# Performance work log

Hardware: AMD Instinct MI355X
Metric: run time of the kernel (lower is better)

Reference implementation:

```python
import jax, jax.numpy as jnp
import numpy as np

V, D, H, S = 100000, 300, 300, 4096   # vocab, embed dim, biLSTM hidden (2x150), seq len
HU = H // 2                            # per-direction LSTM units
NSYN = 4


def _lstm(x, W, U, b):
    """Keras-style LSTM scan. x: [S, D] -> hidden states [S, HU]. Gate order i,f,g,o."""
    def step(carry, xt):
        h, c = carry
        z = xt @ W + h @ U + b              # [4*HU]
        i, f, g, o = jnp.split(z, 4)
        i = jax.nn.sigmoid(i)
        f = jax.nn.sigmoid(f)
        g = jnp.tanh(g)
        o = jax.nn.sigmoid(o)
        c = f * c + i * g
        h = o * jnp.tanh(c)
        return (h, c), h
    init = (jnp.zeros((HU,), x.dtype), jnp.zeros((HU,), x.dtype))
    _, hs = jax.lax.scan(step, init, x)
    return hs


def setup_inputs() -> dict:
    key = jax.random.key(0)
    ks = jax.random.split(key, 20)
    s = 0.05  # small init scale keeps exp() attention scores well-conditioned
    return {
        "sentence": jax.random.randint(ks[0], (S,), 0, V),
        "synonym_indices": jax.random.randint(ks[1], (S, NSYN), 0, V),
        "embedding_matrix": jax.random.normal(ks[2], (V, D), jnp.float32) * s,
        # forward-direction LSTM
        "W_f": jax.random.normal(ks[3], (D, 4 * HU), jnp.float32) * s,
        "U_f": jax.random.normal(ks[4], (HU, 4 * HU), jnp.float32) * s,
        "b_f": jnp.zeros((4 * HU,), jnp.float32),
        # backward-direction LSTM
        "W_b": jax.random.normal(ks[5], (D, 4 * HU), jnp.float32) * s,
        "U_b": jax.random.normal(ks[6], (HU, 4 * HU), jnp.float32) * s,
        "b_b": jnp.zeros((4 * HU,), jnp.float32),
        # primary attention dense (h1 -> h1)
        "W_p": jax.random.normal(ks[7], (H, H), jnp.float32) * s,
        "b_p": jnp.zeros((H,), jnp.float32),
        # secondary attention dense (2*h1 -> 1, tanh)
        "W_s": jax.random.normal(ks[8], (2 * H, 1), jnp.float32) * s,
        "b_s": jnp.zeros((1,), jnp.float32),
        # output heads
        "W_emo": jax.random.normal(ks[9], (2 * H, 8), jnp.float32) * s,
        "b_emo": jnp.zeros((8,), jnp.float32),
        "W_sent": jax.random.normal(ks[10], (2 * H, 1), jnp.float32) * s,
        "b_sent": jnp.zeros((1,), jnp.float32),
    }


def reference(sentence, synonym_indices, embedding_matrix,
              W_f, U_f, b_f, W_b, U_b, b_b,
              W_p, b_p, W_s, b_s, W_emo, b_emo, W_sent, b_sent):
    emb = embedding_matrix[sentence]                       # [S, D] gather
    # bidirectional LSTM (concat fwd and reversed-bwd hidden states)
    h_fwd = _lstm(emb, W_f, U_f, b_f)                      # [S, HU]
    h_bwd = _lstm(emb[::-1], W_b, U_b, b_b)[::-1]          # [S, HU]
    hidden_states = jnp.concatenate([h_fwd, h_bwd], -1)    # [S, H]
    # primary attention: per-word synonym gather + exp-scored weighted sum (vectorized)
    out = hidden_states @ W_p + b_p                        # [S, H]
    syn = embedding_matrix[synonym_indices]                # [S, NSYN, D] irregular gather
    scores = jnp.exp(jnp.einsum('sd,skd->sk', out, syn))   # [S, NSYN]
    m = jnp.einsum('sk,skd->sd', scores, syn)              # [S, D]
    h_hats = jnp.concatenate([hidden_states, m], -1)       # [S, 2H]
    # secondary attention
    coeff = jnp.exp(jnp.tanh(h_hats @ W_s + b_s))          # [S, 1]
    H_HAT = jnp.sum(coeff * h_hats, axis=0)[None, :]       # [1, 2H]
    emotion_logits = H_HAT @ W_emo + b_emo                 # [1, 8]
    sentiment_logits = H_HAT @ W_sent + b_sent             # [1, 1]
    return (emotion_logits, sentiment_logits)
```

## Files before the change

kernel.cpp:

```cpp
#include <hip/hip_runtime.h>
#include <hip/hip_bf16.h>
#include <math.h>

#define S_LEN 4096
#define D_EMB 300
#define NG    600
#define HDIM  300
#define H2    600
#define VOCAB 100000

typedef float v4f __attribute__((ext_vector_type(4)));
typedef _Float16 f16x2 __attribute__((ext_vector_type(2)));
typedef _Float16 f16x8 __attribute__((ext_vector_type(8)));

__device__ __forceinline__ float bf2f(unsigned short u) {
  union { unsigned int i; float f; } v; v.i = ((unsigned int)u) << 16; return v.f;
}
__device__ __forceinline__ unsigned short f2bf(float f) {
  union { float f; unsigned int i; } v; v.f = f;
  return (unsigned short)((v.i + 0x7FFFu + ((v.i >> 16) & 1u)) >> 16);
}

__device__ __forceinline__ void bar_lds() {
  asm volatile("s_waitcnt lgkmcnt(0)\n\ts_barrier" ::: "memory");
}

__global__ void zero_hh(float* __restrict__ HH) {
  if (threadIdx.x < 640) HH[threadIdx.x] = 0.f;
}
__global__ void zero_out_f(float* __restrict__ o, int n) {
  if ((int)threadIdx.x < n) o[threadIdx.x] = 0.f;
}

#define BM 64
#define BN 64
#define BK 16
template<bool A_BF16>
__global__ __launch_bounds__(256) void gemm_bias(
    const void* __restrict__ Av,
    const int* __restrict__ idx, int lda, int nrowsA,
    const float* __restrict__ B,
    const float* __restrict__ bias,
    unsigned short* __restrict__ C,
    int N, int K)
{
  __shared__ __align__(16) float As[BK][BM + 4];
  __shared__ __align__(16) float Bs[BK][BN + 4];
  __shared__ int rowidx[BM];

  int tid = threadIdx.x;
  int bm0 = blockIdx.y * BM, bn0 = blockIdx.x * BN;
  if (tid < BM) {
    int r = idx ? idx[bm0 + tid] : (bm0 + tid);
    r = (r < 0) ? 0 : ((r >= nrowsA) ? (nrowsA - 1) : r);
    rowidx[tid] = r;
  }
  __syncthreads();

  int tx  = tid & 15, ty = tid >> 4;
  int ar  = tid >> 2, akv = (tid & 3) << 2;
  int bkr = tid >> 4, bnv = (tid & 15) << 2;

  float acc[4][4] = {};
  for (int kk = 0; kk < K; kk += BK) {
    float a0=0.f, a1=0.f, a2=0.f, a3=0.f;
    int ka = kk + akv;
    if (ka < K) {
      if (A_BF16) {
        const unsigned short* A = (const unsigned short*)Av;
        ushort4 qa = *(const ushort4*)(A + (size_t)rowidx[ar]*lda + ka);
        a0 = bf2f(qa.x); a1 = bf2f(qa.y); a2 = bf2f(qa.z); a3 = bf2f(qa.w);
      } else {
        const float* A = (const float*)Av;
        float4 qa = *(const float4*)(A + (size_t)rowidx[ar]*lda + ka);
        a0 = qa.x; a1 = qa.y; a2 = qa.z; a3 = qa.w;
      }
    }
    float b0=0.f, b1=0.f, b2=0.f, b3=0.f;
    int kb = kk + bkr, nb = bn0 + bnv;
    if (kb < K && nb < N) {
      float4 qb = *(const float4*)(B + (size_t)kb*N + nb);
      b0 = qb.x; b1 = qb.y; b2 = qb.z; b3 = qb.w;
    }
    As[akv+0][ar] = a0; As[akv+1][ar] = a1; As[akv+2][ar] = a2; As[akv+3][ar] = a3;
    Bs[bkr][bnv+0] = b0; Bs[bkr][bnv+1] = b1; Bs[bkr][bnv+2] = b2; Bs[bkr][bnv+3] = b3;
    __syncthreads();
    #pragma unroll
    for (int k = 0; k < BK; ++k) {
      v4f av = *(const v4f*)&As[k][ty << 2];
      v4f bv = *(const v4f*)&Bs[k][tx << 2];
      #pragma unroll
      for (int i = 0; i < 4; ++i)
        #pragma unroll
        for (int j = 0; j < 4; ++j)
          acc[i][j] += av[i] * bv[j];
    }
    __syncthreads();
  }
  #pragma unroll
  for (int i = 0; i < 4; ++i) {
    int m = bm0 + (ty << 2) + i;
    #pragma unroll
    for (int j = 0; j < 4; ++j) {
      int n = bn0 + (tx << 2) + j;
      if (n < N) C[(size_t)m*N + n] = f2bf(acc[i][j] + bias[n]);
    }
  }
}

__global__ __launch_bounds__(768) void lstm_kernel(
    const unsigned short* __restrict__ pre_f, const unsigned short* __restrict__ pre_b,
    const float* __restrict__ Uf, const float* __restrict__ Ub,
    unsigned short* __restrict__ hidden )
{
  const int dir = blockIdx.x;
  const unsigned short* pre = dir ? pre_b : pre_f;
  const float* U            = dir ? Ub : Uf;
  const int tid = threadIdx.x;

  __shared__ __align__(16) unsigned short h_u16[160];
  __shared__ __align__(16) float z2[3000];
  __shared__ __align__(16) unsigned short h_hist[8][160];

  const bool faP = tid < 750;
  const bool bc  = tid < 150;
  const int c4 = tid % 150, q = tid / 150;
  const int j0 = c4 << 2;
  const int k0 = q << 5;

  f16x2 u[4][16];
  if (faP) {
    #pragma unroll
    for (int cc = 0; cc < 4; ++cc)
      #pragma unroll
      for (int p = 0; p < 16; ++p) {
        int k = k0 + (p << 1);
        float a = (k     < 150) ? U[(size_t)k    *600 + j0 + cc] : 0.f;
        float b = (k + 1 < 150) ? U[(size_t)(k+1)*600 + j0 + cc] : 0.f;
        f16x2 v; v[0] = (_Float16)a; v[1] = (_Float16)b;
        u[cc][p] = v;
      }
  }

  const int t0 = dir ? (S_LEN - 1) : 0;
  const int dt = dir ? -1 : 1;
  const ptrdiff_t pstep = (ptrdiff_t)dt * 600;

  if (tid < 160) h_u16[tid] = 0;

  float pA0=0,pA1=0,pA2=0,pA3=0, pB0=0,pB1=0,pB2=0,pB3=0;
  const unsigned short* pre2 = pre + (ptrdiff_t)t0*600 + 2*pstep;
  if (bc) {
    const unsigned short* g0 = pre + (ptrdiff_t)t0*600;
    pA0 = bf2f(g0[tid]); pA1 = bf2f(g0[tid+150]);
    pA2 = bf2f(g0[tid+300]); pA3 = bf2f(g0[tid+450]);
    const unsigned short* g1 = g0 + pstep;
    pB0 = bf2f(g1[tid]); pB1 = bf2f(g1[tid+150]);
    pB2 = bf2f(g1[tid+300]); pB3 = bf2f(g1[tid+450]);
  }
  float c = 0.f;
  __syncthreads();

  const _Float16* hf = (const _Float16*)h_u16;

  for (int s8 = 0; s8 < S_LEN/8; ++s8) {
    if (s8 && tid < 600) {
      int sub = tid / 75, w = (tid % 75) << 1;
      int sp  = (s8 << 3) - 8 + sub;
      int tp  = dir ? (S_LEN - 1 - sp) : sp;
      *(unsigned int*)(hidden + (size_t)tp*300 + dir*150 + w) =
          *(const unsigned int*)&h_hist[sub][w];
    }
    #pragma unroll
    for (int ss = 0; ss < 8; ++ss) {
      const int s = (s8 << 3) + ss;
      if (faP) {
        f16x2 hp[16];
        *(f16x8*)&hp[0]  = *(const f16x8*)&hf[k0];
        *(f16x8*)&hp[4]  = *(const f16x8*)&hf[k0 + 8];
        *(f16x8*)&hp[8]  = *(const f16x8*)&hf[k0 + 16];
        *(f16x8*)&hp[12] = *(const f16x8*)&hf[k0 + 24];
        float a0 = 0.f, a1 = 0.f, a2 = 0.f, a3 = 0.f;
        #pragma unroll
        for (int p = 0; p < 16; ++p) {
          a0 = __builtin_amdgcn_fdot2(hp[p], u[0][p], a0, false);
          a1 = __builtin_amdgcn_fdot2(hp[p], u[1][p], a1, false);
          a2 = __builtin_amdgcn_fdot2(hp[p], u[2][p], a2, false);
          a3 = __builtin_amdgcn_fdot2(hp[p], u[3][p], a3, false);
        }
        v4f zp; zp[0] = a0; zp[1] = a1; zp[2] = a2; zp[3] = a3;
        *(v4f*)&z2[q*600 + j0] = zp;
      }
      float pC0=0,pC1=0,pC2=0,pC3=0;
      if (bc && s + 2 < S_LEN) {
        pC0 = bf2f(pre2[tid]);       pC1 = bf2f(pre2[tid+150]);
        pC2 = bf2f(pre2[tid+300]);   pC3 = bf2f(pre2[tid+450]);
      }
      bar_lds();

      if (bc) {
        float zi = pA0 + ((z2[tid      ] + z2[600+tid      ]) + (z2[1200+tid      ] + z2[1800+tid      ])) + z2[2400+tid      ];
        float zf = pA1 + ((z2[tid + 150] + z2[600+tid + 150]) + (z2[1200+tid + 150] + z2[1800+tid + 150])) + z2[2400+tid + 150];
        float zg = pA2 + ((z2[tid + 300] + z2[600+tid + 300]) + (z2[1200+tid + 300] + z2[1800+tid + 300])) + z2[2400+tid + 300];
        float zo = pA3 + ((z2[tid + 450] + z2[600+tid + 450]) + (z2[1200+tid + 450] + z2[1800+tid + 450])) + z2[2400+tid + 450];
        float gi = __builtin_amdgcn_rcpf(1.f + __expf(-zi));
        float gf = __builtin_amdgcn_rcpf(1.f + __expf(-zf));
        float gg = 1.f - 2.f * __builtin_amdgcn_rcpf(__expf(2.f * zg) + 1.f);
        float go = __builtin_amdgcn_rcpf(1.f + __expf(-zo));
        c = gf * c + gi * gg;
        float th = 1.f - 2.f * __builtin_amdgcn_rcpf(__expf(2.f * c) + 1.f);
        float hv = go * th;
        ((_Float16*)h_u16)[tid] = (_Float16)hv;
        h_hist[ss][tid] = f2bf(hv);
        pA0 = pB0; pA1 = pB1; pA2 = pB2; pA3 = pB3;
        pB0 = pC0; pB1 = pC1; pB2 = pC2; pB3 = pC3;
      }
      bar_lds();
      pre2 += pstep;
    }
  }

  if (tid < 600) {
    int sub = tid / 75, w = (tid % 75) << 1;
    int sp  = S_LEN - 8 + sub;
    int tp  = dir ? (S_LEN - 1 - sp) : sp;
    *(unsigned int*)(hidden + (size_t)tp*300 + dir*150 + w) =
        *(const unsigned int*)&h_hist[sub][w];
  }
}

__global__ __launch_bounds__(128) void attn_word(
    const unsigned short* __restrict__ outp,
    const unsigned short* __restrict__ hid,
    const float* __restrict__ E,
    const int* __restrict__ syn,
    const float* __restrict__ W_s,
    const float* __restrict__ b_s,
    float* __restrict__ HH)
{
  int t = blockIdx.x, tid = threadIdx.x;
  __shared__ float s_out[300], s_hid[300], s_syn[4][300], s_m[300];
  __shared__ float s_red[8], s_sc[4], s_cf;

  int r0 = syn[t*4+0], r1 = syn[t*4+1], r2 = syn[t*4+2], r3 = syn[t*4+3];
  r0 = (r0 < 0) ? 0 : ((r0 >= VOCAB) ? VOCAB-1 : r0);
  r1 = (r1 < 0) ? 0 : ((r1 >= VOCAB) ? VOCAB-1 : r1);
  r2 = (r2 < 0) ? 0 : ((r2 >= VOCAB) ? VOCAB-1 : r2);
  r3 = (r3 < 0) ? 0 : ((r3 >= VOCAB) ? VOCAB-1 : r3);
  for (int d = tid; d < 300; d += 128) {
    s_out[d] = bf2f(outp[(size_t)t*300 + d]);
    s_hid[d] = bf2f(hid[(size_t)t*300 + d]);
    s_syn[0][d] = E[(size_t)r0*300 + d];
    s_syn[1][d] = E[(size_t)r1*300 + d];
    s_syn[2][d] = E[(size_t)r2*300 + d];
    s_syn[3][d] = E[(size_t)r3*300 + d];
  }
  __syncthreads();

  float p0=0.f, p1=0.f, p2=0.f, p3=0.f;
  for (int d = tid; d < 300; d += 128) {
    float o = s_out[d];
    p0 += o*s_syn[0][d]; p1 += o*s_syn[1][d];
    p2 += o*s_syn[2][d]; p3 += o*s_syn[3][d];
  }
  #pragma unroll
  for (int off = 32; off; off >>= 1) {
    p0 += __shfl_down(p0, off); p1 += __shfl_down(p1, off);
    p2 += __shfl_down(p2, off); p3 += __shfl_down(p3, off);
  }
  int wave = tid >> 6, lane = tid & 63;
  if (lane == 0) {
    s_red[wave*4+0] = p0; s_red[wave*4+1] = p1;
    s_red[wave*4+2] = p2; s_red[wave*4+3] = p3;
  }
  __syncthreads();
  if (tid < 4) s_sc[tid] = __expf(fminf(s_red[tid] + s_red[4 + tid], 50.f));
  __syncthreads();

  float sc0 = s_sc[0], sc1 = s_sc[1], sc2 = s_sc[2], sc3 = s_sc[3];
  float cp = 0.f;
  for (int d = tid; d < 300; d += 128) {
    float m = sc0*s_syn[0][d] + sc1*s_syn[1][d] + sc2*s_syn[2][d] + sc3*s_syn[3][d];
    s_m[d] = m;
    cp += s_hid[d]*W_s[d] + m*W_s[300 + d];
  }
  #pragma unroll
  for (int off = 32; off; off >>= 1) cp += __shfl_down(cp, off);
  if (lane == 0) s_red[wave] = cp;
  __syncthreads();
  if (tid == 0) s_cf = __expf(tanhf(s_red[0] + s_red[1] + b_s[0]));
  __syncthreads();

  float cf = s_cf;
  for (int d = tid; d < 300; d += 128) {
    atomicAdd(&HH[d],       cf * s_hid[d]);
    atomicAdd(&HH[300 + d], cf * s_m[d]);
  }
}

__global__ void heads(const float* __restrict__ HH,
                      const float* __restrict__ W_emo, const float* __restrict__ b_emo,
                      const float* __restrict__ W_sent, const float* __restrict__ b_sent,
                      float* __restrict__ out) {
  int tid = threadIdx.x;
  if (tid < 8) {
    float a = 0.f;
    for (int d = 0; d < H2; ++d) a += HH[d] * W_emo[d*8 + tid];
    out[tid] = a + b_emo[tid];
  } else if (tid == 8) {
    float a = 0.f;
    for (int d = 0; d < H2; ++d) a += HH[d] * W_sent[d];
    out[8] = a + b_sent[0];
  }
}

extern "C" void kernel_launch(void* const* d_in, const int* in_sizes, int n_in,
                              void* d_out, int out_size, void* d_ws, size_t ws_size,
                              hipStream_t stream) {
  const int*   sentence = (const int*)d_in[0];
  const int*   syn_idx  = (const int*)d_in[1];
  const float* E        = (const float*)d_in[2];
  const float* W_f      = (const float*)d_in[3];
  const float* U_f      = (const float*)d_in[4];
  const float* b_f      = (const float*)d_in[5];
  const float* W_b      = (const float*)d_in[6];
  const float* U_b      = (const float*)d_in[7];
  const float* b_b      = (const float*)d_in[8];
  const float* W_p      = (const float*)d_in[9];
  const float* b_p      = (const float*)d_in[10];
  const float* W_s      = (const float*)d_in[11];
  const float* b_s      = (const float*)d_in[12];
  const float* W_emo    = (const float*)d_in[13];
  const float* b_emo    = (const float*)d_in[14];
  const float* W_sent   = (const float*)d_in[15];
  const float* b_sent   = (const float*)d_in[16];
  float*       outv     = (float*)d_out;

  unsigned char* ws = (unsigned char*)d_ws;
  float*          HH     = (float*)ws;
  unsigned short* hidden = (unsigned short*)(ws + 2560);
  unsigned short* out_p  = (unsigned short*)(ws + 2460160);
  unsigned short* pre_f  = (unsigned short*)(ws + 4917760);
  unsigned short* pre_b  = (unsigned short*)(ws + 9832960);

  if (ws_size < 14748160u) {
    zero_out_f<<<1, 64, 0, stream>>>(outv, out_size);
    return;
  }

  zero_hh<<<1, 640, 0, stream>>>(HH);
  gemm_bias<false><<<dim3(10, 64), 256, 0, stream>>>(
      (const void*)E, sentence, D_EMB, VOCAB, W_f, b_f, pre_f, NG, D_EMB);
  gemm_bias<false><<<dim3(10, 64), 256, 0, stream>>>(
      (const void*)E, sentence, D_EMB, VOCAB, W_b, b_b, pre_b, NG, D_EMB);
  lstm_kernel<<<2, 768, 0, stream>>>(pre_f, pre_b, U_f, U_b, hidden);
  gemm_bias<true><<<dim3(5, 64), 256, 0, stream>>>(
      (const void*)hidden, nullptr, HDIM, S_LEN, W_p, b_p, out_p, HDIM, HDIM);
  attn_word<<<S_LEN, 128, 0, stream>>>(out_p, hidden, E, syn_idx, W_s, b_s, HH);
  heads<<<1, 64, 0, stream>>>(HH, W_emo, b_emo, W_sent, b_sent, outv);
}
```

Measured before the change: 3.643 ms.

## Assign one LSTM gate column per thread and compute activations in parallel

The recurrent matvec is re-partitioned. Previously 750 threads each computed a partial K-slice for four columns, and 150 threads reduced five partials per gate. Now each of 600 threads owns one full gate column, with 80 fp16 pairs of U held in registers, so no split-K reduction through LDS is needed. Each thread also applies its own sigmoid or tanh activation before writing G, which spreads the transcendental work across 600 lanes instead of 150. The cost is a longer serial dot product per thread (80 fdot2 versus 16×4) and higher register pressure.

```diff
diff --git a/kernel.cpp b/kernel.cpp
--- a/kernel.cpp
+++ b/kernel.cpp
@@ -108,7 +108,7 @@
   }
 }
 
-__global__ __launch_bounds__(768) void lstm_kernel(
+__global__ __launch_bounds__(640) void lstm_kernel(
     const unsigned short* __restrict__ pre_f, const unsigned short* __restrict__ pre_b,
     const float* __restrict__ Uf, const float* __restrict__ Ub,
     unsigned short* __restrict__ hidden )
@@ -119,44 +119,39 @@
   const int tid = threadIdx.x;
 
   __shared__ __align__(16) unsigned short h_u16[160];
-  __shared__ __align__(16) float z2[3000];
+  __shared__ __align__(16) float G[600];
   __shared__ __align__(16) unsigned short h_hist[8][160];
 
-  const bool faP = tid < 750;
-  const bool bc  = tid < 150;
-  const int c4 = tid % 150, q = tid / 150;
-  const int j0 = c4 << 2;
-  const int k0 = q << 5;
-
-  f16x2 u[4][16];
-  if (faP) {
+  const bool colT = tid < 600;
+  const bool bc   = tid < 150;
+  const int  j    = tid;
+  const bool is_g = (j >= 300) && (j < 450);
+  const float gm  = is_g ?  2.f : -1.f;
+  const float gya = is_g ? -2.f :  1.f;
+  const float gyb = is_g ?  1.f :  0.f;
+
+  f16x2 u[80];
+  if (colT) {
     #pragma unroll
-    for (int cc = 0; cc < 4; ++cc)
-      #pragma unroll
-      for (int p = 0; p < 16; ++p) {
-        int k = k0 + (p << 1);
-        float a = (k     < 150) ? U[(size_t)k    *600 + j0 + cc] : 0.f;
-        float b = (k + 1 < 150) ? U[(size_t)(k+1)*600 + j0 + cc] : 0.f;
-        f16x2 v; v[0] = (_Float16)a; v[1] = (_Float16)b;
-        u[cc][p] = v;
-      }
+    for (int p = 0; p < 80; ++p) {
+      int k = p << 1;
+      float a = (k     < 150) ? U[(size_t)k    *600 + j] : 0.f;
+      float b = (k + 1 < 150) ? U[(size_t)(k+1)*600 + j] : 0.f;
+      f16x2 v; v[0] = (_Float16)a; v[1] = (_Float16)b;
+      u[p] = v;
+    }
   }
 
   const int t0 = dir ? (S_LEN - 1) : 0;
-  const int dt = dir ? -1 : 1;
-  const ptrdiff_t pstep = (ptrdiff_t)dt * 600;
+  const ptrdiff_t pstep = (ptrdiff_t)(dir ? -1 : 1) * 600;
 
   if (tid < 160) h_u16[tid] = 0;
 
-  float pA0=0,pA1=0,pA2=0,pA3=0, pB0=0,pB1=0,pB2=0,pB3=0;
+  float pA = 0.f, pB = 0.f;
   const unsigned short* pre2 = pre + (ptrdiff_t)t0*600 + 2*pstep;
-  if (bc) {
-    const unsigned short* g0 = pre + (ptrdiff_t)t0*600;
-    pA0 = bf2f(g0[tid]); pA1 = bf2f(g0[tid+150]);
-    pA2 = bf2f(g0[tid+300]); pA3 = bf2f(g0[tid+450]);
-    const unsigned short* g1 = g0 + pstep;
-    pB0 = bf2f(g1[tid]); pB1 = bf2f(g1[tid+150]);
-    pB2 = bf2f(g1[tid+300]); pB3 = bf2f(g1[tid+450]);
+  if (colT) {
+    pA = bf2f(pre[(ptrdiff_t)t0*600 + j]);
+    pB = bf2f(pre[(ptrdiff_t)t0*600 + pstep + j]);
   }
   float c = 0.f;
   __syncthreads();
@@ -174,46 +169,39 @@
     #pragma unroll
     for (int ss = 0; ss < 8; ++ss) {
       const int s = (s8 << 3) + ss;
-      if (faP) {
-        f16x2 hp[16];
-        *(f16x8*)&hp[0]  = *(const f16x8*)&hf[k0];
-        *(f16x8*)&hp[4]  = *(const f16x8*)&hf[k0 + 8];
-        *(f16x8*)&hp[8]  = *(const f16x8*)&hf[k0 + 16];
-        *(f16x8*)&hp[12] = *(const f16x8*)&hf[k0 + 24];
+      float pC = 0.f;
+      if (colT) {
+        if (s + 2 < S_LEN) pC = bf2f(pre2[j]);
         float a0 = 0.f, a1 = 0.f, a2 = 0.f, a3 = 0.f;
         #pragma unroll
-        for (int p = 0; p < 16; ++p) {
-          a0 = __builtin_amdgcn_fdot2(hp[p], u[0][p], a0, false);
-          a1 = __builtin_amdgcn_fdot2(hp[p], u[1][p], a1, false);
-          a2 = __builtin_amdgcn_fdot2(hp[p], u[2][p], a2, false);
-          a3 = __builtin_amdgcn_fdot2(hp[p], u[3][p], a3, false);
+        for (int cc = 0; cc < 5; ++cc) {
+          f16x2 hp[16];
+          *(f16x8*)&hp[0]  = *(const f16x8*)&hf[cc*32];
+          *(f16x8*)&hp[4]  = *(const f16x8*)&hf[cc*32 + 8];
+          *(f16x8*)&hp[8]  = *(const f16x8*)&hf[cc*32 + 16];
+          *(f16x8*)&hp[12] = *(const f16x8*)&hf[cc*32 + 24];
+          #pragma unroll
+          for (int p = 0; p < 16; p += 4) {
+            a0 = __builtin_amdgcn_fdot2(hp[p+0], u[cc*16 + p+0], a0, false);
+            a1 = __builtin_amdgcn_fdot2(hp[p+1], u[cc*16 + p+1], a1, false);
+            a2 = __builtin_amdgcn_fdot2(hp[p+2], u[cc*16 + p+2], a2, false);
+            a3 = __builtin_amdgcn_fdot2(hp[p+3], u[cc*16 + p+3], a3, false);
+          }
         }
-        v4f zp; zp[0] = a0; zp[1] = a1; zp[2] = a2; zp[3] = a3;
-        *(v4f*)&z2[q*600 + j0] = zp;
-      }
-      float pC0=0,pC1=0,pC2=0,pC3=0;
-      if (bc && s + 2 < S_LEN) {
-        pC0 = bf2f(pre2[tid]);       pC1 = bf2f(pre2[tid+150]);
-        pC2 = bf2f(pre2[tid+300]);   pC3 = bf2f(pre2[tid+450]);
+        float z = pA + ((a0 + a1) + (a2 + a3));
+        float y = __builtin_amdgcn_rcpf(1.f + __expf(gm * z));
+        G[j] = fmaf(gya, y, gyb);
+        pA = pB; pB = pC;
       }
       bar_lds();
 
       if (bc) {
-        float zi = pA0 + ((z2[tid      ] + z2[600+tid      ]) + (z2[1200+tid      ] + z2[1800+tid      ])) + z2[2400+tid      ];
-        float zf = pA1 + ((z2[tid + 150] + z2[600+tid + 150]) + (z2[1200+tid + 150] + z2[1800+tid + 150])) + z2[2400+tid + 150];
-        float zg = pA2 + ((z2[tid + 300] + z2[600+tid + 300]) + (z2[1200+tid + 300] + z2[1800+tid + 300])) + z2[2400+tid + 300];
-        float zo = pA3 + ((z2[tid + 450] + z2[600+tid + 450]) + (z2[1200+tid + 450] + z2[1800+tid + 450])) + z2[2400+tid + 450];
-        float gi = __builtin_amdgcn_rcpf(1.f + __expf(-zi));
-        float gf = __builtin_amdgcn_rcpf(1.f + __expf(-zf));
-        float gg = 1.f - 2.f * __builtin_amdgcn_rcpf(__expf(2.f * zg) + 1.f);
-        float go = __builtin_amdgcn_rcpf(1.f + __expf(-zo));
+        float gi = G[tid], gf = G[150 + tid], gg = G[300 + tid], go = G[450 + tid];
         c = gf * c + gi * gg;
         float th = 1.f - 2.f * __builtin_amdgcn_rcpf(__expf(2.f * c) + 1.f);
         float hv = go * th;
         ((_Float16*)h_u16)[tid] = (_Float16)hv;
         h_hist[ss][tid] = f2bf(hv);
-        pA0 = pB0; pA1 = pB1; pA2 = pB2; pA3 = pB3;
-        pB0 = pC0; pB1 = pC1; pB2 = pC2; pB3 = pC3;
       }
       bar_lds();
       pre2 += pstep;
@@ -353,7 +341,7 @@
       (const void*)E, sentence, D_EMB, VOCAB, W_f, b_f, pre_f, NG, D_EMB);
   gemm_bias<false><<<dim3(10, 64), 256, 0, stream>>>(
       (const void*)E, sentence, D_EMB, VOCAB, W_b, b_b, pre_b, NG, D_EMB);
-  lstm_kernel<<<2, 768, 0, stream>>>(pre_f, pre_b, U_f, U_b, hidden);
+  lstm_kernel<<<2, 640, 0, stream>>>(pre_f, pre_b, U_f, U_b, hidden);
   gemm_bias<true><<<dim3(5, 64), 256, 0, stream>>>(
       (const void*)hidden, nullptr, HDIM, S_LEN, W_p, b_p, out_p, HDIM, HDIM);
   attn_word<<<S_LEN, 128, 0, stream>>>(out_p, hidden, E, syn_idx, W_s, b_s, HH);
```

Measured after the change: 4.092 ms. +12.3%, slower.

## Spread LSTM gate activations across 600 threads with extra LDS stage

Applied to the files above, without the earlier changes.

Gate pre-activation reduction and sigmoid/tanh evaluation now run on 600 threads, one gate element each, instead of 150 threads each computing four gates. Results go to a new shared array G, and the 150 cell threads then read them to update c and h. Each thread also prefetches one pre-activation value instead of four. The serial per-step critical path through the activations gets shorter, at the cost of a third barrier per timestep in a latency-bound recurrence.

```diff
diff --git a/kernel.cpp b/kernel.cpp
--- a/kernel.cpp
+++ b/kernel.cpp
@@ -120,13 +120,20 @@
 
   __shared__ __align__(16) unsigned short h_u16[160];
   __shared__ __align__(16) float z2[3000];
+  __shared__ __align__(16) float G[600];
   __shared__ __align__(16) unsigned short h_hist[8][160];
 
-  const bool faP = tid < 750;
-  const bool bc  = tid < 150;
+  const bool faP  = tid < 750;
+  const bool actT = tid < 600;
+  const bool bc   = tid < 150;
   const int c4 = tid % 150, q = tid / 150;
   const int j0 = c4 << 2;
   const int k0 = q << 5;
+
+  const bool is_g = (tid >= 300) && (tid < 450);
+  const float gm  = is_g ?  2.f : -1.f;
+  const float gya = is_g ? -2.f :  1.f;
+  const float gyb = is_g ?  1.f :  0.f;
 
   f16x2 u[4][16];
   if (faP) {
@@ -148,15 +155,12 @@
 
   if (tid < 160) h_u16[tid] = 0;
 
-  float pA0=0,pA1=0,pA2=0,pA3=0, pB0=0,pB1=0,pB2=0,pB3=0;
+  float pA = 0.f, pB = 0.f;
   const unsigned short* pre2 = pre + (ptrdiff_t)t0*600 + 2*pstep;
-  if (bc) {
+  if (actT) {
     const unsigned short* g0 = pre + (ptrdiff_t)t0*600;
-    pA0 = bf2f(g0[tid]); pA1 = bf2f(g0[tid+150]);
-    pA2 = bf2f(g0[tid+300]); pA3 = bf2f(g0[tid+450]);
-    const unsigned short* g1 = g0 + pstep;
-    pB0 = bf2f(g1[tid]); pB1 = bf2f(g1[tid+150]);
-    pB2 = bf2f(g1[tid+300]); pB3 = bf2f(g1[tid+450]);
+    pA = bf2f(g0[tid]);
+    pB = bf2f(g0[pstep + tid]);
   }
   float c = 0.f;
   __syncthreads();
@@ -174,6 +178,8 @@
     #pragma unroll
     for (int ss = 0; ss < 8; ++ss) {
       const int s = (s8 << 3) + ss;
+      unsigned short pCr = 0;
+      if (actT && s + 2 < S_LEN) pCr = pre2[tid];
       if (faP) {
         f16x2 hp[16];
         *(f16x8*)&hp[0]  = *(const f16x8*)&hf[k0];
@@ -191,29 +197,24 @@
         v4f zp; zp[0] = a0; zp[1] = a1; zp[2] = a2; zp[3] = a3;
         *(v4f*)&z2[q*600 + j0] = zp;
       }
-      float pC0=0,pC1=0,pC2=0,pC3=0;
-      if (bc && s + 2 < S_LEN) {
-        pC0 = bf2f(pre2[tid]);       pC1 = bf2f(pre2[tid+150]);
-        pC2 = bf2f(pre2[tid+300]);   pC3 = bf2f(pre2[tid+450]);
-      }
       bar_lds();
 
+      if (actT) {
+        float z = pA + ((z2[tid] + z2[600 + tid]) + (z2[1200 + tid] + z2[1800 + tid]))
+                     + z2[2400 + tid];
+        float y = __builtin_amdgcn_rcpf(1.f + __expf(gm * z));
+        G[tid] = fmaf(gya, y, gyb);
+        pA = pB; pB = bf2f(pCr);
+      }
+      bar_lds();
+
       if (bc) {
-        float zi = pA0 + ((z2[tid      ] + z2[600+tid      ]) + (z2[1200+tid      ] + z2[1800+tid      ])) + z2[2400+tid      ];
-        float zf = pA1 + ((z2[tid + 150] + z2[600+tid + 150]) + (z2[1200+tid + 150] + z2[1800+tid + 150])) + z2[2400+tid + 150];
-        float zg = pA2 + ((z2[tid + 300] + z2[600+tid + 300]) + (z2[1200+tid + 300] + z2[1800+tid + 300])) + z2[2400+tid + 300];
-        float zo = pA3 + ((z2[tid + 450] + z2[600+tid + 450]) + (z2[1200+tid + 450] + z2[1800+tid + 450])) + z2[2400+tid + 450];
-        float gi = __builtin_amdgcn_rcpf(1.f + __expf(-zi));
-        float gf = __builtin_amdgcn_rcpf(1.f + __expf(-zf));
-        float gg = 1.f - 2.f * __builtin_amdgcn_rcpf(__expf(2.f * zg) + 1.f);
-        float go = __builtin_amdgcn_rcpf(1.f + __expf(-zo));
+        float gi = G[tid], gf = G[150 + tid], gg = G[300 + tid], go = G[450 + tid];
         c = gf * c + gi * gg;
         float th = 1.f - 2.f * __builtin_amdgcn_rcpf(__expf(2.f * c) + 1.f);
         float hv = go * th;
         ((_Float16*)h_u16)[tid] = (_Float16)hv;
         h_hist[ss][tid] = f2bf(hv);
-        pA0 = pB0; pA1 = pB1; pA2 = pB2; pA3 = pB3;
-        pB0 = pC0; pB1 = pC1; pB2 = pC2; pB3 = pC3;
       }
       bar_lds();
       pre2 += pstep;
```

Result: slower. 4.605 ms (+26.4%).

## Compute LSTM recurrent matvec with MFMA instead of fdot2 partial sums

Applied to the files above, without the earlier changes.

Replaces the per-step recurrent h@U product, previously split over 750 threads with fdot2 and a 5-way partial-sum reduction in shared memory, with 16x16x32 f16 MFMA instructions. U is held in registers as MFMA B fragments across 10 waves, and only one output row of each tile is written to shared memory. This removes the cross-thread reduction and shrinks the LDS traffic on the serial critical path. The cost is that 15 of the 16 MFMA rows do redundant work, and the block drops to 640 threads.

```diff
diff --git a/kernel.cpp b/kernel.cpp
--- a/kernel.cpp
+++ b/kernel.cpp
@@ -108,7 +108,7 @@
   }
 }
 
-__global__ __launch_bounds__(768) void lstm_kernel(
+__global__ __launch_bounds__(640) void lstm_kernel(
     const unsigned short* __restrict__ pre_f, const unsigned short* __restrict__ pre_b,
     const float* __restrict__ Uf, const float* __restrict__ Ub,
     unsigned short* __restrict__ hidden )
@@ -116,30 +116,36 @@
   const int dir = blockIdx.x;
   const unsigned short* pre = dir ? pre_b : pre_f;
   const float* U            = dir ? Ub : Uf;
-  const int tid = threadIdx.x;
+  const int tid  = threadIdx.x;
+  const int wave = tid >> 6, lane = tid & 63;
 
   __shared__ __align__(16) unsigned short h_u16[160];
-  __shared__ __align__(16) float z2[3000];
+  __shared__ __align__(16) float zrow[608];
   __shared__ __align__(16) unsigned short h_hist[8][160];
 
-  const bool faP = tid < 750;
-  const bool bc  = tid < 150;
-  const int c4 = tid % 150, q = tid / 150;
-  const int j0 = c4 << 2;
-  const int k0 = q << 5;
-
-  f16x2 u[4][16];
-  if (faP) {
+  const bool bc = tid < 150;
+
+  const int ncnt   = (wave < 2) ? 3 : 4;
+  const int nstart = (wave < 2) ? 3 * wave : 6 + 4 * (wave - 2);
+
+  const int bgrp = lane >> 4;
+  const int bn   = lane & 15;
+
+  f16x8 bfr[4][5];
+  #pragma unroll
+  for (int t = 0; t < 4; ++t) {
     #pragma unroll
-    for (int cc = 0; cc < 4; ++cc)
+    for (int kt = 0; kt < 5; ++kt) {
+      f16x8 v;
       #pragma unroll
-      for (int p = 0; p < 16; ++p) {
-        int k = k0 + (p << 1);
-        float a = (k     < 150) ? U[(size_t)k    *600 + j0 + cc] : 0.f;
-        float b = (k + 1 < 150) ? U[(size_t)(k+1)*600 + j0 + cc] : 0.f;
-        f16x2 v; v[0] = (_Float16)a; v[1] = (_Float16)b;
-        u[cc][p] = v;
-      }
+      for (int e = 0; e < 8; ++e) {
+        int row = (kt << 5) + (bgrp << 3) + e;
+        int col = ((nstart + t) << 4) + bn;
+        float x = (t < ncnt && row < 150 && col < 600) ? U[(size_t)row*600 + col] : 0.f;
+        v[e] = (_Float16)x;
+      }
+      bfr[t][kt] = v;
+    }
   }
 
   const int t0 = dir ? (S_LEN - 1) : 0;
@@ -174,37 +180,39 @@
     #pragma unroll
     for (int ss = 0; ss < 8; ++ss) {
       const int s = (s8 << 3) + ss;
-      if (faP) {
-        f16x2 hp[16];
-        *(f16x8*)&hp[0]  = *(const f16x8*)&hf[k0];
-        *(f16x8*)&hp[4]  = *(const f16x8*)&hf[k0 + 8];
-        *(f16x8*)&hp[8]  = *(const f16x8*)&hf[k0 + 16];
-        *(f16x8*)&hp[12] = *(const f16x8*)&hf[k0 + 24];
-        float a0 = 0.f, a1 = 0.f, a2 = 0.f, a3 = 0.f;
-        #pragma unroll
-        for (int p = 0; p < 16; ++p) {
-          a0 = __builtin_amdgcn_fdot2(hp[p], u[0][p], a0, false);
-          a1 = __builtin_amdgcn_fdot2(hp[p], u[1][p], a1, false);
-          a2 = __builtin_amdgcn_fdot2(hp[p], u[2][p], a2, false);
-          a3 = __builtin_amdgcn_fdot2(hp[p], u[3][p], a3, false);
-        }
-        v4f zp; zp[0] = a0; zp[1] = a1; zp[2] = a2; zp[3] = a3;
-        *(v4f*)&z2[q*600 + j0] = zp;
-      }
       float pC0=0,pC1=0,pC2=0,pC3=0;
       if (bc && s + 2 < S_LEN) {
         pC0 = bf2f(pre2[tid]);       pC1 = bf2f(pre2[tid+150]);
         pC2 = bf2f(pre2[tid+300]);   pC3 = bf2f(pre2[tid+450]);
       }
+      {
+        v4f a0 = {0.f,0.f,0.f,0.f}, a1 = a0, a2 = a0, a3 = a0;
+        #pragma unroll
+        for (int kt = 0; kt < 5; ++kt) {
+          f16x8 av = *(const f16x8*)&hf[(kt << 5) + (bgrp << 3)];
+          a0 = __builtin_amdgcn_mfma_f32_16x16x32_f16(av, bfr[0][kt], a0, 0, 0, 0);
+          a1 = __builtin_amdgcn_mfma_f32_16x16x32_f16(av, bfr[1][kt], a1, 0, 0, 0);
+          a2 = __builtin_amdgcn_mfma_f32_16x16x32_f16(av, bfr[2][kt], a2, 0, 0, 0);
+          if (ncnt == 4)
+            a3 = __builtin_amdgcn_mfma_f32_16x16x32_f16(av, bfr[3][kt], a3, 0, 0, 0);
+        }
+        if (lane < 16) {
+          int base = (nstart << 4) + bn;
+          zrow[base]      = a0[0];
+          zrow[base + 16] = a1[0];
+          zrow[base + 32] = a2[0];
+          if (ncnt == 4) zrow[base + 48] = a3[0];
+        }
+      }
       bar_lds();
 
       if (bc) {
-        float zi = pA0 + ((z2[tid      ] + z2[600+tid      ]) + (z2[1200+tid      ] + z2[1800+tid      ])) + z2[2400+tid      ];
-        float zf = pA1 + ((z2[tid + 150] + z2[600+tid + 150]) + (z2[1200+tid + 150] + z2[1800+tid + 150])) + z2[2400+tid + 150];
-        float zg = pA2 + ((z2[tid + 300] + z2[600+tid + 300]) + (z2[1200+tid + 300] + z2[1800+tid + 300])) + z2[2400+tid + 300];
-        float zo = pA3 + ((z2[tid + 450] + z2[600+tid + 450]) + (z2[1200+tid + 450] + z2[1800+tid + 450])) + z2[2400+tid + 450];
+        float zi = pA0 + zrow[tid];
+        float zff= pA1 + zrow[150 + tid];
+        float zg = pA2 + zrow[300 + tid];
+        float zo = pA3 + zrow[450 + tid];
         float gi = __builtin_amdgcn_rcpf(1.f + __expf(-zi));
-        float gf = __builtin_amdgcn_rcpf(1.f + __expf(-zf));
+        float gf = __builtin_amdgcn_rcpf(1.f + __expf(-zff));
         float gg = 1.f - 2.f * __builtin_amdgcn_rcpf(__expf(2.f * zg) + 1.f);
         float go = __builtin_amdgcn_rcpf(1.f + __expf(-zo));
         c = gf * c + gi * gg;
@@ -353,7 +361,7 @@
       (const void*)E, sentence, D_EMB, VOCAB, W_f, b_f, pre_f, NG, D_EMB);
   gemm_bias<false><<<dim3(10, 64), 256, 0, stream>>>(
       (const void*)E, sentence, D_EMB, VOCAB, W_b, b_b, pre_b, NG, D_EMB);
-  lstm_kernel<<<2, 768, 0, stream>>>(pre_f, pre_b, U_f, U_b, hidden);
+  lstm_kernel<<<2, 640, 0, stream>>>(pre_f, pre_b, U_f, U_b, hidden);
   gemm_bias<true><<<dim3(5, 64), 256, 0, stream>>>(
       (const void*)hidden, nullptr, HDIM, S_LEN, W_p, b_p, out_p, HDIM, HDIM);
   attn_word<<<S_LEN, 128, 0, stream>>>(out_p, hidden, E, syn_idx, W_s, b_s, HH);
```

After: 3.740 ms. 2.6% more time.
